# Kernel tuning notes

Measured on AMD Instinct MI355X. Metric: run time of the kernel, lower is better.

The kernel has to match this reference:

```python
import math
import jax, jax.numpy as jnp
import numpy as np

CAPACITY_FACTOR = 1.25  # _DEFAULT_EP_CAPACITY_FACTOR
STD = 0.02


def setup_inputs() -> dict:
    key = jax.random.key(0)
    k_x, k_r, k_ug, k_d = jax.random.split(key, 4)
    B, S, D, E, I = 8, 4096, 1024, 16, 2816
    x = jax.random.normal(k_x, (B, S, D), dtype=jnp.float32)
    router = STD * jax.random.truncated_normal(k_r, -3, 3, (D, E)).astype(jnp.float32)
    w_up_gate = STD * jax.random.truncated_normal(k_ug, -3, 3, (E, D, 2 * I)).astype(jnp.float32)
    w_down = STD * jax.random.truncated_normal(k_d, -3, 3, (E, I, D)).astype(jnp.float32)
    return {"x": x, "router": router, "w_up_gate": w_up_gate, "w_down": w_down,
            "num_experts_per_token": 2}


def _routing_stats(selected_experts, router_probs, router_logits, num_experts, k):
    probs = router_probs.astype(jnp.float32)
    logits = router_logits.astype(jnp.float32)
    expert_counts = jnp.sum(jax.nn.one_hot(selected_experts, num_experts, dtype=jnp.float32), axis=(0, 1))
    total = jnp.maximum(jnp.sum(expert_counts), 1.0)
    frac = expert_counts / total
    entropy = -jnp.sum(frac * jnp.log(frac + 1e-06))
    token_fraction = frac * k
    p = jnp.mean(probs, axis=0)
    lb_loss = num_experts * jnp.sum(token_fraction * p)
    z = jax.scipy.special.logsumexp(logits, axis=-1)
    z_loss = jnp.mean(z ** 2)
    return expert_counts, entropy, lb_loss, z_loss


def _moe_forward(x, router, w_up_gate, w_down, k):
    B, S, D = x.shape
    E = router.shape[1]
    T = B * S
    x_flat = x.reshape(T, D)

    router_logits = jnp.einsum('td,de->te', x_flat, router)          # [T,E]
    router_probs = jax.nn.softmax(router_logits, axis=-1)
    topk_logits, selected = jax.lax.top_k(router_logits, k)          # [T,K]
    combine = jax.nn.softmax(topk_logits, axis=-1).astype(x.dtype)   # [T,K]

    stats = _routing_stats(selected, router_probs, router_logits, E, k)

    # ---- capacity-based dispatch ----
    C = int(math.ceil(T * k / E * CAPACITY_FACTOR))                  # static
    TK = T * k
    flat_sel = selected.reshape(TK).astype(jnp.int32)                # token-major priority
    oh = jax.nn.one_hot(flat_sel, E, dtype=jnp.int32)                # [TK,E]
    pos = jnp.take_along_axis(jnp.cumsum(oh, axis=0), flat_sel[:, None], axis=1)[:, 0] - 1
    keep = pos < C                                                   # [TK]
    pos_safe = jnp.where(keep, pos, 0)
    token_idx = jnp.arange(TK, dtype=jnp.int32) // k

    vals = jnp.where(keep[:, None], x_flat[token_idx], 0.0)          # [TK,D]
    expert_in = jnp.zeros((E, C, D), dtype=x.dtype).at[flat_sel, pos_safe].add(vals)

    # ---- grouped SwiGLU MLP ----
    h = jnp.einsum('ecd,edf->ecf', expert_in, w_up_gate)             # [E,C,2I]
    I = w_down.shape[1]
    gate, up = h[..., :I], h[..., I:]
    act = jax.nn.silu(gate) * up                                     # [E,C,I]
    expert_out = jnp.einsum('eci,eid->ecd', act, w_down)             # [E,C,D]

    # ---- combine ----
    gathered = expert_out[flat_sel, pos_safe]                        # [TK,D]
    w = (combine.reshape(TK) * keep.astype(x.dtype))[:, None]
    routed = (gathered * w).reshape(T, k, D).sum(axis=1)             # [T,D]
    return routed.reshape(B, S, D), stats


def reference(x, router, w_up_gate, w_down, num_experts_per_token):
    routed, (counts, entropy, lb_loss, z_loss) = _moe_forward(
        x, router, w_up_gate, w_down, num_experts_per_token)
    return routed, counts, entropy, lb_loss, z_loss
```

## Files before the change

### kernel.cpp

```cpp
#include <hip/hip_runtime.h>
#include <math.h>

#define T_TOK 32768
#define TKA   65536
#define DIM   1024
#define NE    16
#define IDIM  2816
#define CAP   5120

typedef short short8 __attribute__((ext_vector_type(8)));
typedef float floatx4 __attribute__((ext_vector_type(4)));

__device__ __forceinline__ unsigned short f2bf(float f) {
  unsigned int u = __float_as_uint(f);
  u = u + 0x7FFFu + ((u >> 16) & 1u);
  return (unsigned short)(u >> 16);
}
__device__ __forceinline__ float bf2f(unsigned short h) {
  return __uint_as_float(((unsigned int)h) << 16);
}

__device__ __forceinline__ void gld_lds16(const void* g, void* l) {
  __builtin_amdgcn_global_load_lds(
      (const __attribute__((address_space(1))) unsigned int*)(unsigned long long)g,
      (__attribute__((address_space(3))) unsigned int*)(unsigned int)(unsigned long long)l,
      16, 0, 0);
}


__global__ void cvtx_kernel(const float* __restrict__ in, unsigned short* __restrict__ out) {
  size_t i = ((size_t)blockIdx.x * 256 + threadIdx.x) * 8;
  float4 a = *(const float4*)(in + i);
  float4 b = *(const float4*)(in + i + 4);
  short8 v;
  v[0] = (short)f2bf(a.x); v[1] = (short)f2bf(a.y); v[2] = (short)f2bf(a.z); v[3] = (short)f2bf(a.w);
  v[4] = (short)f2bf(b.x); v[5] = (short)f2bf(b.y); v[6] = (short)f2bf(b.z); v[7] = (short)f2bf(b.w);
  *(short8*)(out + i) = v;
}

__global__ void transpose_cvt(const float* __restrict__ in, unsigned short* __restrict__ out,
                              int R, int Cin) {
  int e = blockIdx.z;
  size_t base = (size_t)e * R * Cin;
  int ct = blockIdx.x;
  int rt = blockIdx.y;
  __shared__ unsigned short Ts[64][72];
  int tx = threadIdx.x & 63, ty = threadIdx.x >> 6;
#pragma unroll
  for (int j = 0; j < 16; j++) {
    int r = rt * 64 + ty + j * 4;
    int c = ct * 64 + tx;
    Ts[tx][ty + j * 4] = f2bf(in[base + (size_t)r * Cin + c]);
  }
  __syncthreads();
#pragma unroll
  for (int j = 0; j < 16; j++) {
    int cl = ty + j * 4;
    out[base + (size_t)(ct * 64 + cl) * R + rt * 64 + tx] = Ts[cl][tx];
  }
}


__global__ void router_kernel(const float* __restrict__ x, const float* __restrict__ router,
                              float* __restrict__ logits) {
  int tid = blockIdx.x * 256 + threadIdx.x;
  int tk = tid >> 4, e = tid & 15;
  const float* xr = x + (size_t)tk * DIM;
  float acc = 0.f;
#pragma unroll 8
  for (int d = 0; d < DIM; d++) acc = fmaf(xr[d], router[d * NE + e], acc);
  logits[tid] = acc;
}

__global__ void topk_kernel(const float* __restrict__ logits, int* __restrict__ sel,
                            float* __restrict__ wcomb, float* __restrict__ prob_sums,
                            int* __restrict__ counts_raw, float* __restrict__ z2sum) {
  __shared__ float ps[16];
  __shared__ int   cs[16];
  __shared__ float zs;
  int tid = threadIdx.x;
  if (tid < 16) { ps[tid] = 0.f; cs[tid] = 0; }
  if (tid == 0) zs = 0.f;
  __syncthreads();
  int t = blockIdx.x * 256 + tid;
  float l[16];
#pragma unroll
  for (int e = 0; e < 16; e++) l[e] = logits[(size_t)t * 16 + e];
  float m1 = l[0]; int e1 = 0;
#pragma unroll
  for (int e = 1; e < 16; e++) if (l[e] > m1) { m1 = l[e]; e1 = e; }
  float m2 = -3.4e38f; int e2 = 0;
#pragma unroll
  for (int e = 0; e < 16; e++) if (e != e1 && l[e] > m2) { m2 = l[e]; e2 = e; }
  float b  = __expf(m2 - m1);
  float w1 = 1.f / (1.f + b);
  sel[t * 2] = e1; sel[t * 2 + 1] = e2;
  wcomb[t * 2] = w1; wcomb[t * 2 + 1] = 1.f - w1;
  float s = 0.f;
  float pexp[16];
#pragma unroll
  for (int e = 0; e < 16; e++) { pexp[e] = __expf(l[e] - m1); s += pexp[e]; }
  float inv = 1.f / s;
#pragma unroll
  for (int e = 0; e < 16; e++) atomicAdd(&ps[e], pexp[e] * inv);
  atomicAdd(&cs[e1], 1); atomicAdd(&cs[e2], 1);
  float z = m1 + __logf(s);
  atomicAdd(&zs, z * z);
  __syncthreads();
  if (tid < 16) { atomicAdd(&prob_sums[tid], ps[tid]); atomicAdd(&counts_raw[tid], cs[tid]); }
  if (tid == 0) atomicAdd(z2sum, zs);
}

__global__ void hist_kernel(const int* __restrict__ sel, int* __restrict__ bhist) {
  __shared__ int h[16];
  int tid = threadIdx.x;
  if (tid < 16) h[tid] = 0;
  __syncthreads();
  atomicAdd(&h[sel[blockIdx.x * 256 + tid]], 1);
  __syncthreads();
  if (tid < 16) bhist[blockIdx.x * 16 + tid] = h[tid];
}

__global__ void scan_kernel(const int* __restrict__ bhist, int* __restrict__ bbase,
                            int* __restrict__ capc) {
  int e = threadIdx.x;
  if (e >= 16) return;
  int run = 0;
  for (int b = 0; b < 256; b++) { bbase[b * 16 + e] = run; run += bhist[b * 16 + e]; }
  capc[e] = run < CAP ? run : CAP;
}

__global__ void rank_kernel(const int* __restrict__ sel, const int* __restrict__ bbase,
                            int* __restrict__ pos_tk, int* __restrict__ scat) {
  __shared__ int se[256];
  int i = threadIdx.x;
  int a = blockIdx.x * 256 + i;
  int e = sel[a];
  se[i] = e;
  __syncthreads();
  int r = 0;
  for (int j = 0; j < i; j++) r += (se[j] == e) ? 1 : 0;
  int pos = bbase[blockIdx.x * 16 + e] + r;
  if (pos < CAP) { pos_tk[a] = pos; scat[e * CAP + pos] = a >> 1; }
  else           { pos_tk[a] = -1; }
}


__global__ __launch_bounds__(256) void gemm1_kernel(
    const unsigned short* __restrict__ xb, const unsigned short* __restrict__ wtg,
    const int* __restrict__ scat, const int* __restrict__ capc,
    const unsigned short* __restrict__ zrow, unsigned short* __restrict__ act) {
  int e = blockIdx.z, ct = blockIdx.x, it = blockIdx.y;
  if (ct * 128 >= capc[e]) return;
  __shared__ __align__(16) unsigned short As[128 * 32];
  __shared__ __align__(16) unsigned short Bg[64 * 32];
  __shared__ __align__(16) unsigned short Bu[64 * 32];
  const int t = threadIdx.x, w = t >> 6, l = t & 63;
  const int lq = l >> 4, koff = (l & 3) * 8, lr = l >> 2;

  const unsigned short *arow0, *arow1;
  {
    int c0 = ct * 128 + w * 32 + lr;
    int tok0 = scat[e * CAP + c0];
    int tok1 = scat[e * CAP + c0 + 16];
    arow0 = (tok0 >= 0 ? xb + (size_t)tok0 * DIM : zrow) + koff;
    arow1 = (tok1 >= 0 ? xb + (size_t)tok1 * DIM : zrow) + koff;
  }
  const unsigned short* bgrow =
      wtg + ((size_t)e * (2 * IDIM) + (size_t)(it * 64 + w * 16 + lr)) * DIM + koff;
  const unsigned short* burow = bgrow + (size_t)IDIM * DIM;

  void* adst0 = (char*)As + w * 2048;
  void* adst1 = (char*)As + w * 2048 + 1024;
  void* bgdst = (char*)Bg + w * 1024;
  void* budst = (char*)Bu + w * 1024;

  floatx4 accg[8], accu[8];
#pragma unroll
  for (int i = 0; i < 8; i++) {
    accg[i] = (floatx4){0.f, 0.f, 0.f, 0.f};
    accu[i] = (floatx4){0.f, 0.f, 0.f, 0.f};
  }
  const int wm = w >> 1, wn = w & 1;
  const int am = wm * 64 + (l & 15);
  const int bn = wn * 32 + (l & 15);

  for (int k0 = 0; k0 < DIM; k0 += 32) {
    __syncthreads();
    gld_lds16(arow0 + k0, adst0);
    gld_lds16(arow1 + k0, adst1);
    gld_lds16(bgrow + k0, bgdst);
    gld_lds16(burow + k0, budst);
    __syncthreads();
    short8 af[4], bgf[2], buf2[2];
#pragma unroll
    for (int mi = 0; mi < 4; mi++)
      af[mi] = *(const short8*)(As + (am + mi * 16) * 32 + lq * 8);
#pragma unroll
    for (int ni = 0; ni < 2; ni++) {
      bgf[ni]  = *(const short8*)(Bg + (bn + ni * 16) * 32 + lq * 8);
      buf2[ni] = *(const short8*)(Bu + (bn + ni * 16) * 32 + lq * 8);
    }
#pragma unroll
    for (int mi = 0; mi < 4; mi++)
#pragma unroll
      for (int ni = 0; ni < 2; ni++) {
        accg[mi * 2 + ni] = __builtin_amdgcn_mfma_f32_16x16x32_bf16(af[mi], bgf[ni],  accg[mi * 2 + ni], 0, 0, 0);
        accu[mi * 2 + ni] = __builtin_amdgcn_mfma_f32_16x16x32_bf16(af[mi], buf2[ni], accu[mi * 2 + ni], 0, 0, 0);
      }
  }

  size_t abase = ((size_t)e * CAP + (size_t)ct * 128) * IDIM + (size_t)it * 64;
#pragma unroll
  for (int mi = 0; mi < 4; mi++)
#pragma unroll
    for (int reg = 0; reg < 4; reg++) {
      int m = wm * 64 + mi * 16 + lq * 4 + reg;
#pragma unroll
      for (int ni = 0; ni < 2; ni++) {
        int n = wn * 32 + ni * 16 + (l & 15);
        float g = accg[mi * 2 + ni][reg];
        float u = accu[mi * 2 + ni][reg];
        float a = g / (1.f + __expf(-g)) * u;
        act[abase + (size_t)m * IDIM + n] = f2bf(a);
      }
    }
}


__global__ __launch_bounds__(256) void gemm2_kernel(
    const unsigned short* __restrict__ act, const unsigned short* __restrict__ wtd,
    const int* __restrict__ capc, unsigned short* __restrict__ eout) {
  int e = blockIdx.z, ct = blockIdx.x, it = blockIdx.y;
  if (ct * 128 >= capc[e]) return;
  __shared__ __align__(16) unsigned short As[128 * 32];
  __shared__ __align__(16) unsigned short Bs[64 * 32];
  const int t = threadIdx.x, w = t >> 6, l = t & 63;
  const int lq = l >> 4, koff = (l & 3) * 8, lr = l >> 2;

  const unsigned short* arow0 = act + ((size_t)e * CAP + ct * 128 + w * 32 + lr) * IDIM + koff;
  const unsigned short* arow1 = arow0 + (size_t)16 * IDIM;
  const unsigned short* brow  = wtd + ((size_t)e * DIM + it * 64 + w * 16 + lr) * IDIM + koff;

  void* adst0 = (char*)As + w * 2048;
  void* adst1 = (char*)As + w * 2048 + 1024;
  void* bdst  = (char*)Bs + w * 1024;

  floatx4 acc[8];
#pragma unroll
  for (int i = 0; i < 8; i++) acc[i] = (floatx4){0.f, 0.f, 0.f, 0.f};
  const int wm = w >> 1, wn = w & 1;
  const int am = wm * 64 + (l & 15);
  const int bn = wn * 32 + (l & 15);

  for (int k0 = 0; k0 < IDIM; k0 += 32) {
    __syncthreads();
    gld_lds16(arow0 + k0, adst0);
    gld_lds16(arow1 + k0, adst1);
    gld_lds16(brow + k0, bdst);
    __syncthreads();
    short8 af[4], bf2[2];
#pragma unroll
    for (int mi = 0; mi < 4; mi++)
      af[mi] = *(const short8*)(As + (am + mi * 16) * 32 + lq * 8);
#pragma unroll
    for (int ni = 0; ni < 2; ni++)
      bf2[ni] = *(const short8*)(Bs + (bn + ni * 16) * 32 + lq * 8);
#pragma unroll
    for (int mi = 0; mi < 4; mi++)
#pragma unroll
      for (int ni = 0; ni < 2; ni++)
        acc[mi * 2 + ni] = __builtin_amdgcn_mfma_f32_16x16x32_bf16(af[mi], bf2[ni], acc[mi * 2 + ni], 0, 0, 0);
  }

  size_t obase = ((size_t)e * CAP + (size_t)ct * 128) * DIM + (size_t)it * 64;
#pragma unroll
  for (int mi = 0; mi < 4; mi++)
#pragma unroll
    for (int reg = 0; reg < 4; reg++) {
      int m = wm * 64 + mi * 16 + lq * 4 + reg;
#pragma unroll
      for (int ni = 0; ni < 2; ni++) {
        int n = wn * 32 + ni * 16 + (l & 15);
        eout[obase + (size_t)m * DIM + n] = f2bf(acc[mi * 2 + ni][reg]);
      }
    }
}


__global__ void combine_kernel(const unsigned short* __restrict__ eout,
                               const int* __restrict__ sel, const int* __restrict__ pos_tk,
                               const float* __restrict__ wcomb, float* __restrict__ routed) {
  int tok = blockIdx.x;
  int d = threadIdx.x * 4;
  float a0 = 0.f, a1 = 0.f, a2 = 0.f, a3 = 0.f;
#pragma unroll
  for (int s = 0; s < 2; s++) {
    int a = tok * 2 + s;
    int p = pos_tk[a];
    if (p >= 0) {
      int e = sel[a];
      float wgt = wcomb[a];
      const unsigned short* row = eout + ((size_t)e * CAP + p) * DIM + d;
      ushort4 r = *(const ushort4*)row;
      a0 += wgt * bf2f(r.x); a1 += wgt * bf2f(r.y);
      a2 += wgt * bf2f(r.z); a3 += wgt * bf2f(r.w);
    }
  }
  float4 o = {a0, a1, a2, a3};
  *(float4*)(routed + (size_t)tok * DIM + d) = o;
}

__global__ void finalize_kernel(const int* __restrict__ counts_raw, const float* __restrict__ psums,
                                const float* __restrict__ z2sum, float* __restrict__ tail) {
  if (threadIdx.x != 0 || blockIdx.x != 0) return;
  float ent = 0.f, lb = 0.f;
  for (int e = 0; e < 16; e++) {
    float c = (float)counts_raw[e];
    tail[e] = c;
    float frac = c / 65536.f;
    ent -= frac * logf(frac + 1e-6f);
    lb += frac * 2.f * (psums[e] / 32768.f);
  }
  tail[16] = ent;
  tail[17] = 16.f * lb;
  tail[18] = z2sum[0] / 32768.f;
}


extern "C" void kernel_launch(void* const* d_in, const int* in_sizes, int n_in,
                              void* d_out, int out_size, void* d_ws, size_t ws_size,
                              hipStream_t stream) {
  (void)in_sizes; (void)n_in; (void)out_size; (void)ws_size;
  const float* x         = (const float*)d_in[0];
  const float* router    = (const float*)d_in[1];
  const float* w_up_gate = (const float*)d_in[2];
  const float* w_down    = (const float*)d_in[3];
  float* out = (float*)d_out;

  char* p = (char*)d_ws;
  size_t off = 0;
  auto alc = [&](size_t n) { void* r = p + off; off += (n + 255) & ~(size_t)255; return r; };

  unsigned short* xb   = (unsigned short*)alc((size_t)T_TOK * DIM * 2);
  unsigned short* wtg  = (unsigned short*)alc((size_t)NE * 2 * IDIM * DIM * 2);
  unsigned short* wtd  = (unsigned short*)alc((size_t)NE * DIM * IDIM * 2);
  unsigned short* act  = (unsigned short*)alc((size_t)NE * CAP * IDIM * 2);
  unsigned short* eout = (unsigned short*)alc((size_t)NE * CAP * DIM * 2);
  float* logits = (float*)alc((size_t)T_TOK * NE * 4);
  int*   sel    = (int*)alc((size_t)TKA * 4);
  float* wcomb  = (float*)alc((size_t)TKA * 4);
  int*   pos_tk = (int*)alc((size_t)TKA * 4);
  int*   scat   = (int*)alc((size_t)NE * CAP * 4);
  int*   bhist  = (int*)alc(256 * 16 * 4);
  int*   bbase  = (int*)alc(256 * 16 * 4);
  int*   capc   = (int*)alc(64);
  int*   counts_raw = (int*)alc(64);
  float* psums  = (float*)alc(64);
  float* z2     = (float*)alc(64);
  unsigned short* zrow = (unsigned short*)alc(DIM * 2);

  hipMemsetAsync(counts_raw, 0, 64, stream);
  hipMemsetAsync(psums, 0, 64, stream);
  hipMemsetAsync(z2, 0, 64, stream);
  hipMemsetAsync(scat, 0xFF, (size_t)NE * CAP * 4, stream);
  hipMemsetAsync(zrow, 0, DIM * 2, stream);

  cvtx_kernel<<<T_TOK * DIM / (256 * 8), 256, 0, stream>>>(x, xb);
  transpose_cvt<<<dim3(2 * IDIM / 64, DIM / 64, NE), 256, 0, stream>>>(w_up_gate, wtg, DIM, 2 * IDIM);
  transpose_cvt<<<dim3(DIM / 64, IDIM / 64, NE), 256, 0, stream>>>(w_down, wtd, IDIM, DIM);

  router_kernel<<<T_TOK * NE / 256, 256, 0, stream>>>(x, router, logits);
  topk_kernel<<<T_TOK / 256, 256, 0, stream>>>(logits, sel, wcomb, psums, counts_raw, z2);
  hist_kernel<<<TKA / 256, 256, 0, stream>>>(sel, bhist);
  scan_kernel<<<1, 64, 0, stream>>>(bhist, bbase, capc);
  rank_kernel<<<TKA / 256, 256, 0, stream>>>(sel, bbase, pos_tk, scat);

  gemm1_kernel<<<dim3(CAP / 128, IDIM / 64, NE), 256, 0, stream>>>(xb, wtg, scat, capc, zrow, act);
  gemm2_kernel<<<dim3(CAP / 128, DIM / 64, NE), 256, 0, stream>>>(act, wtd, capc, eout);

  combine_kernel<<<T_TOK, 256, 0, stream>>>(eout, sel, pos_tk, wcomb, out);
  finalize_kernel<<<1, 64, 0, stream>>>(counts_raw, psums, z2, out + (size_t)T_TOK * DIM);
}
```

Baseline: 2.700 ms.

## Double K-tile depth to 64 and XOR-swizzle LDS layout in both expert GEMMs

Both grouped GEMM kernels now stage a 64-wide K slice per iteration instead of 32. This halves the number of barrier pairs and load rounds per output tile. The LDS layout uses an XOR swizzle of the 16-byte chunk index by row, applied consistently on the global-to-LDS writes and the fragment reads, to avoid bank conflicts on the wider rows. In exchange LDS usage per block doubles, which may reduce occupancy, and there is still no double-buffering.

Result: faster. 2.482 ms (-8.1%).

```diff
diff --git a/kernel.cpp b/kernel.cpp
--- a/kernel.cpp
+++ b/kernel.cpp
@@ -152,28 +152,28 @@
     const unsigned short* __restrict__ zrow, unsigned short* __restrict__ act) {
   int e = blockIdx.z, ct = blockIdx.x, it = blockIdx.y;
   if (ct * 128 >= capc[e]) return;
-  __shared__ __align__(16) unsigned short As[128 * 32];
-  __shared__ __align__(16) unsigned short Bg[64 * 32];
-  __shared__ __align__(16) unsigned short Bu[64 * 32];
+  __shared__ __align__(16) unsigned short As[128 * 64];
+  __shared__ __align__(16) unsigned short Bg[64 * 64];
+  __shared__ __align__(16) unsigned short Bu[64 * 64];
   const int t = threadIdx.x, w = t >> 6, l = t & 63;
-  const int lq = l >> 4, koff = (l & 3) * 8, lr = l >> 2;
-
-  const unsigned short *arow0, *arow1;
-  {
-    int c0 = ct * 128 + w * 32 + lr;
-    int tok0 = scat[e * CAP + c0];
-    int tok1 = scat[e * CAP + c0 + 16];
-    arow0 = (tok0 >= 0 ? xb + (size_t)tok0 * DIM : zrow) + koff;
-    arow1 = (tok1 >= 0 ? xb + (size_t)tok1 * DIM : zrow) + koff;
-  }
-  const unsigned short* bgrow =
-      wtg + ((size_t)e * (2 * IDIM) + (size_t)(it * 64 + w * 16 + lr)) * DIM + koff;
-  const unsigned short* burow = bgrow + (size_t)IDIM * DIM;
-
-  void* adst0 = (char*)As + w * 2048;
-  void* adst1 = (char*)As + w * 2048 + 1024;
-  void* bgdst = (char*)Bg + w * 1024;
-  void* budst = (char*)Bu + w * 1024;
+  const int lr8   = l >> 3;
+  const int koffs = ((l & 7) ^ lr8) * 8;
+
+  const unsigned short* aptr[4];
+#pragma unroll
+  for (int j = 0; j < 4; j++) {
+    int c0 = ct * 128 + w * 32 + j * 8 + lr8;
+    int tok = scat[e * CAP + c0];
+    aptr[j] = (tok >= 0 ? xb + (size_t)tok * DIM : zrow) + koffs;
+  }
+  const unsigned short* bgp[2];
+  const unsigned short* bup[2];
+#pragma unroll
+  for (int j = 0; j < 2; j++) {
+    int n0 = it * 64 + w * 16 + j * 8 + lr8;
+    bgp[j] = wtg + ((size_t)e * (2 * IDIM) + n0) * DIM + koffs;
+    bup[j] = bgp[j] + (size_t)IDIM * DIM;
+  }
 
   floatx4 accg[8], accu[8];
 #pragma unroll
@@ -182,32 +182,39 @@
     accu[i] = (floatx4){0.f, 0.f, 0.f, 0.f};
   }
   const int wm = w >> 1, wn = w & 1;
-  const int am = wm * 64 + (l & 15);
-  const int bn = wn * 32 + (l & 15);
-
-  for (int k0 = 0; k0 < DIM; k0 += 32) {
+  const int rl = l & 15, lq = l >> 4, sx = l & 7;
+
+  for (int k0 = 0; k0 < DIM; k0 += 64) {
     __syncthreads();
-    gld_lds16(arow0 + k0, adst0);
-    gld_lds16(arow1 + k0, adst1);
-    gld_lds16(bgrow + k0, bgdst);
-    gld_lds16(burow + k0, budst);
+#pragma unroll
+    for (int j = 0; j < 4; j++)
+      gld_lds16(aptr[j] + k0, (char*)As + w * 4096 + j * 1024);
+#pragma unroll
+    for (int j = 0; j < 2; j++) {
+      gld_lds16(bgp[j] + k0, (char*)Bg + w * 2048 + j * 1024);
+      gld_lds16(bup[j] + k0, (char*)Bu + w * 2048 + j * 1024);
+    }
     __syncthreads();
-    short8 af[4], bgf[2], buf2[2];
-#pragma unroll
-    for (int mi = 0; mi < 4; mi++)
-      af[mi] = *(const short8*)(As + (am + mi * 16) * 32 + lq * 8);
-#pragma unroll
-    for (int ni = 0; ni < 2; ni++) {
-      bgf[ni]  = *(const short8*)(Bg + (bn + ni * 16) * 32 + lq * 8);
-      buf2[ni] = *(const short8*)(Bu + (bn + ni * 16) * 32 + lq * 8);
-    }
-#pragma unroll
-    for (int mi = 0; mi < 4; mi++)
+#pragma unroll
+    for (int ks = 0; ks < 2; ks++) {
+      const int slot = ((ks * 4 + lq) ^ sx) * 8;
+      short8 af[4], bgf[2], buf2[2];
+#pragma unroll
+      for (int mi = 0; mi < 4; mi++)
+        af[mi] = *(const short8*)(As + (wm * 64 + mi * 16 + rl) * 64 + slot);
 #pragma unroll
       for (int ni = 0; ni < 2; ni++) {
-        accg[mi * 2 + ni] = __builtin_amdgcn_mfma_f32_16x16x32_bf16(af[mi], bgf[ni],  accg[mi * 2 + ni], 0, 0, 0);
-        accu[mi * 2 + ni] = __builtin_amdgcn_mfma_f32_16x16x32_bf16(af[mi], buf2[ni], accu[mi * 2 + ni], 0, 0, 0);
+        bgf[ni]  = *(const short8*)(Bg + (wn * 32 + ni * 16 + rl) * 64 + slot);
+        buf2[ni] = *(const short8*)(Bu + (wn * 32 + ni * 16 + rl) * 64 + slot);
       }
+#pragma unroll
+      for (int mi = 0; mi < 4; mi++)
+#pragma unroll
+        for (int ni = 0; ni < 2; ni++) {
+          accg[mi * 2 + ni] = __builtin_amdgcn_mfma_f32_16x16x32_bf16(af[mi], bgf[ni],  accg[mi * 2 + ni], 0, 0, 0);
+          accu[mi * 2 + ni] = __builtin_amdgcn_mfma_f32_16x16x32_bf16(af[mi], buf2[ni], accu[mi * 2 + ni], 0, 0, 0);
+        }
+    }
   }
 
   size_t abase = ((size_t)e * CAP + (size_t)ct * 128) * IDIM + (size_t)it * 64;
@@ -233,44 +240,52 @@
     const int* __restrict__ capc, unsigned short* __restrict__ eout) {
   int e = blockIdx.z, ct = blockIdx.x, it = blockIdx.y;
   if (ct * 128 >= capc[e]) return;
-  __shared__ __align__(16) unsigned short As[128 * 32];
-  __shared__ __align__(16) unsigned short Bs[64 * 32];
+  __shared__ __align__(16) unsigned short As[128 * 64];
+  __shared__ __align__(16) unsigned short Bs[64 * 64];
   const int t = threadIdx.x, w = t >> 6, l = t & 63;
-  const int lq = l >> 4, koff = (l & 3) * 8, lr = l >> 2;
-
-  const unsigned short* arow0 = act + ((size_t)e * CAP + ct * 128 + w * 32 + lr) * IDIM + koff;
-  const unsigned short* arow1 = arow0 + (size_t)16 * IDIM;
-  const unsigned short* brow  = wtd + ((size_t)e * DIM + it * 64 + w * 16 + lr) * IDIM + koff;
-
-  void* adst0 = (char*)As + w * 2048;
-  void* adst1 = (char*)As + w * 2048 + 1024;
-  void* bdst  = (char*)Bs + w * 1024;
+  const int lr8   = l >> 3;
+  const int koffs = ((l & 7) ^ lr8) * 8;
+
+  const unsigned short* aptr[4];
+#pragma unroll
+  for (int j = 0; j < 4; j++)
+    aptr[j] = act + ((size_t)e * CAP + ct * 128 + w * 32 + j * 8 + lr8) * IDIM + koffs;
+  const unsigned short* bptr[2];
+#pragma unroll
+  for (int j = 0; j < 2; j++)
+    bptr[j] = wtd + ((size_t)e * DIM + it * 64 + w * 16 + j * 8 + lr8) * IDIM + koffs;
 
   floatx4 acc[8];
 #pragma unroll
   for (int i = 0; i < 8; i++) acc[i] = (floatx4){0.f, 0.f, 0.f, 0.f};
   const int wm = w >> 1, wn = w & 1;
-  const int am = wm * 64 + (l & 15);
-  const int bn = wn * 32 + (l & 15);
-
-  for (int k0 = 0; k0 < IDIM; k0 += 32) {
+  const int rl = l & 15, lq = l >> 4, sx = l & 7;
+
+  for (int k0 = 0; k0 < IDIM; k0 += 64) {
     __syncthreads();
-    gld_lds16(arow0 + k0, adst0);
-    gld_lds16(arow1 + k0, adst1);
-    gld_lds16(brow + k0, bdst);
+#pragma unroll
+    for (int j = 0; j < 4; j++)
+      gld_lds16(aptr[j] + k0, (char*)As + w * 4096 + j * 1024);
+#pragma unroll
+    for (int j = 0; j < 2; j++)
+      gld_lds16(bptr[j] + k0, (char*)Bs + w * 2048 + j * 1024);
     __syncthreads();
-    short8 af[4], bf2[2];
-#pragma unroll
-    for (int mi = 0; mi < 4; mi++)
-      af[mi] = *(const short8*)(As + (am + mi * 16) * 32 + lq * 8);
-#pragma unroll
-    for (int ni = 0; ni < 2; ni++)
-      bf2[ni] = *(const short8*)(Bs + (bn + ni * 16) * 32 + lq * 8);
-#pragma unroll
-    for (int mi = 0; mi < 4; mi++)
+#pragma unroll
+    for (int ks = 0; ks < 2; ks++) {
+      const int slot = ((ks * 4 + lq) ^ sx) * 8;
+      short8 af[4], bf2[2];
+#pragma unroll
+      for (int mi = 0; mi < 4; mi++)
+        af[mi] = *(const short8*)(As + (wm * 64 + mi * 16 + rl) * 64 + slot);
 #pragma unroll
       for (int ni = 0; ni < 2; ni++)
-        acc[mi * 2 + ni] = __builtin_amdgcn_mfma_f32_16x16x32_bf16(af[mi], bf2[ni], acc[mi * 2 + ni], 0, 0, 0);
+        bf2[ni] = *(const short8*)(Bs + (wn * 32 + ni * 16 + rl) * 64 + slot);
+#pragma unroll
+      for (int mi = 0; mi < 4; mi++)
+#pragma unroll
+        for (int ni = 0; ni < 2; ni++)
+          acc[mi * 2 + ni] = __builtin_amdgcn_mfma_f32_16x16x32_bf16(af[mi], bf2[ni], acc[mi * 2 + ni], 0, 0, 0);
+    }
   }
 
   size_t obase = ((size_t)e * CAP + (size_t)ct * 128) * DIM + (size_t)it * 64;
```
